# Optimization experiments

Measured on AMD Instinct MI355X. Metric: run time of the kernel, lower is better.

The kernel has to match this reference:

```python
import jax, jax.numpy as jnp
import numpy as np

B, DIM, NH = 2, 192, 6
HD = DIM // NH
S, H, W = 16, 32, 32
WS = (4, 4, 4)
WN = (S // WS[0], H // WS[1], W // WS[2])  # windows per axis (4,8,8)
NW = WN[0] * WN[1] * WN[2]                 # 256 windows
NWIN = WS[0] * WS[1] * WS[2]               # 64 tokens per window
SCALE = HD ** -0.5
TABLE = (2 * WS[0] - 1) * (2 * WS[1] - 1) * (2 * WS[2] - 1)  # 343


def _static_coords():
    # replicates torch __init__ base_coords / coords (shift_size=0, no padding)
    ls = np.linspace(-1, 1, S); lh = np.linspace(-1, 1, H); lw = np.linspace(-1, 1, W)
    img = np.stack(np.meshgrid(lw, lh, ls, indexing='ij'), 0)   # (3,W,H,S), ch=(x,y,z)
    img = img.transpose(0, 3, 2, 1)                              # (3,S,H,W)
    wr = img.reshape(3, WN[0], WS[0], WN[1], WS[1], WN[2], WS[2]).mean((2, 4, 6))
    wr = wr.reshape(1, 3, WN[0], 1, WN[1], 1, WN[2], 1)
    bs = np.arange(WS[0]) * 2.0 / (S - 1); bs = bs - bs.mean()
    bh = np.arange(WS[1]) * 2.0 / (H - 1); bh = bh - bh.mean()
    bw = np.arange(WS[2]) * 2.0 / (W - 1); bw = bw - bw.mean()
    es = np.tile(bs, WN[0]); eh = np.tile(bh, WN[1]); ew = np.tile(bw, WN[2])
    c = np.stack(np.meshgrid(ew, eh, es, indexing='ij'), 0).transpose(0, 3, 2, 1)
    c = c.reshape(1, 3, WN[0], WS[0], WN[1], WS[1], WN[2], WS[2])
    return (wr + c).astype(np.float32), c.astype(np.float32)

BASE_COORDS, REL_COORDS = _static_coords()


def _rel_pos_index():
    g = np.stack(np.meshgrid(np.arange(WS[0]), np.arange(WS[1]), np.arange(WS[2]), indexing='ij'))
    f = g.reshape(3, -1)
    r = (f[:, :, None] - f[:, None, :]).transpose(1, 2, 0)
    r[..., 0] += WS[0] - 1; r[..., 1] += WS[1] - 1; r[..., 2] += WS[2] - 1
    r[..., 0] *= 3 * WS[1] - 1   # faithful to source (3*ws_h-1 multiplier)
    r[..., 1] *= 2 * WS[1] - 1
    return r.sum(-1)  # (NWIN, NWIN) int

RPI = _rel_pos_index()


def conv1(x, w, b):  # 1x1x1 conv3d
    return jnp.einsum('bcshw,oc->boshw', x, w) + b[None, :, None, None, None]


def avg_pool_win(x):
    return x.reshape(x.shape[0], x.shape[1], WN[0], WS[0], WN[1], WS[1], WN[2], WS[2]).mean((3, 5, 7))


def leaky(x):
    return jnp.where(x >= 0, x, 0.01 * x)


def grid_sample_3d(inp, grid):
    # inp (N,C,D,H,W); grid (N,D,H,W,3) last dim = (x,y,z); align_corners=True, zeros padding
    N, C, D, Hh, Ww = inp.shape
    gx = (grid[..., 0] + 1.0) * (Ww - 1) / 2.0
    gy = (grid[..., 1] + 1.0) * (Hh - 1) / 2.0
    gz = (grid[..., 2] + 1.0) * (D - 1) / 2.0
    x0f = jnp.floor(gx); y0f = jnp.floor(gy); z0f = jnp.floor(gz)
    fx = gx - x0f; fy = gy - y0f; fz = gz - z0f
    x0 = x0f.astype(jnp.int32); y0 = y0f.astype(jnp.int32); z0 = z0f.astype(jnp.int32)

    def gat(iz, iy, ix):
        valid = ((iz >= 0) & (iz < D) & (iy >= 0) & (iy < Hh) & (ix >= 0) & (ix < Ww)).astype(inp.dtype)
        izc = jnp.clip(iz, 0, D - 1); iyc = jnp.clip(iy, 0, Hh - 1); ixc = jnp.clip(ix, 0, Ww - 1)
        vals = jax.vmap(lambda im, a, b, c: im[:, a, b, c])(inp, izc, iyc, ixc)  # (N,C,D,H,W)
        return vals * valid[:, None]

    out = jnp.zeros_like(inp)
    for dz, wz in ((0, 1.0 - fz), (1, fz)):
        for dy, wy in ((0, 1.0 - fy), (1, fy)):
            for dx, wx in ((0, 1.0 - fx), (1, fx)):
                out = out + gat(z0 + dz, y0 + dy, x0 + dx) * (wz * wy * wx)[:, None]
    return out


def to_windows(t):  # (B*NH, HD, S, H, W) -> (B*NW, NH, NWIN, HD)
    t = t.reshape(B, NH, HD, WN[0], WS[0], WN[1], WS[1], WN[2], WS[2])
    t = t.transpose(0, 3, 5, 7, 1, 4, 6, 8, 2)
    return t.reshape(B * NW, NH, NWIN, HD)


def setup_inputs() -> dict:
    key = jax.random.key(0)
    ks = jax.random.split(key, 8)
    return {
        'x': jax.random.normal(ks[0], (B, DIM, S, H, W), jnp.float32),
        'x_up': jax.random.normal(ks[1], (B, DIM, S, H, W), jnp.float32),
        'w_qkv': jax.random.normal(ks[2], (3 * DIM, DIM), jnp.float32) * 0.02,
        'b_qkv': jnp.zeros((3 * DIM,), jnp.float32),
        'w_off': jax.random.normal(ks[3], (NH * 3, DIM), jnp.float32) * 0.02,
        'b_off': jnp.zeros((NH * 3,), jnp.float32),
        'w_scale': jax.random.normal(ks[4], (NH * 3, DIM), jnp.float32) * 0.02,
        'b_scale': jnp.zeros((NH * 3,), jnp.float32),
        'w_proj': jax.random.normal(ks[5], (DIM, DIM), jnp.float32) * 0.02,
        'b_proj': jnp.zeros((DIM,), jnp.float32),
        'rpb_table': jax.random.normal(ks[6], (TABLE, NH), jnp.float32) * 0.02,
    }


def reference(x, x_up, w_qkv, b_qkv, w_off, b_off, w_scale, b_scale, w_proj, b_proj, rpb_table):
    # deformable sampling offsets / scales (avgpool -> leakyrelu -> 1x1 conv3d)
    pooled = leaky(avg_pool_win(x))
    off = conv1(pooled, w_off, b_off).reshape(B * NH, 3, WN[0], WN[1], WN[2])
    div = jnp.array([W // WS[2], H // WS[1], S // WS[0]], dtype=x.dtype).reshape(1, 3, 1, 1, 1)
    off = off / div
    sc = conv1(pooled, w_scale, b_scale).reshape(B * NH, 3, WN[0], WN[1], WN[2])
    coords = (jnp.asarray(BASE_COORDS)
              + jnp.asarray(REL_COORDS) * sc[:, :, :, None, :, None, :, None]
              + off[:, :, :, None, :, None, :, None])
    grid = coords.transpose(0, 2, 3, 4, 5, 6, 7, 1).reshape(B * NH, S, H, W, 3)

    # qkv 1x1 conv3d
    qkv = conv1(x, w_qkv, b_qkv).reshape(B, 3, NH, HD, S, H, W).transpose(1, 0, 2, 3, 4, 5, 6)
    q = qkv[0].reshape(B * NH, HD, S, H, W)
    k = qkv[1].reshape(B * NH, HD, S, H, W)
    v = qkv[2].reshape(B * NH, HD, S, H, W)

    k = grid_sample_3d(k, grid)
    v = grid_sample_3d(v, grid)

    qw, kw, vw = to_windows(q), to_windows(k), to_windows(v)
    rpb = rpb_table[jnp.asarray(RPI.reshape(-1))].reshape(NWIN, NWIN, NH).transpose(2, 0, 1)
    attn = jnp.einsum('wnqd,wnkd->wnqk', qw * SCALE, kw) + rpb[None]
    attn = jax.nn.softmax(attn, axis=-1)
    out = jnp.einsum('wnqk,wnkd->wnqd', attn, vw)

    out = out.reshape(B, WN[0], WN[1], WN[2], NH, WS[0], WS[1], WS[2], HD)
    out = out.transpose(0, 4, 8, 1, 5, 2, 6, 3, 7).reshape(B, DIM, S, H, W)
    return conv1(out, w_proj, b_proj)
```

## Files before the change

### kernel.cpp

```cpp
#include <hip/hip_runtime.h>
#include <math.h>

#define BB    2
#define DIMC  192
#define NHH   6
#define HDD   32
#define NPOS  16384
#define NWTOT 256
#define ATT_SCALE 0.17677669529663687f

typedef _Float16 f16x8 __attribute__((ext_vector_type(8)));
typedef _Float16 f16x4 __attribute__((ext_vector_type(4)));
typedef float f32x4 __attribute__((ext_vector_type(4)));

static __device__ __forceinline__ uint2 shfl_u2(uint2 v, int src) {
  uint2 r;
  r.x = (unsigned)__shfl((int)v.x, src, 64);
  r.y = (unsigned)__shfl((int)v.y, src, 64);
  return r;
}

__global__ void k_prep(const float* __restrict__ wq, const float* __restrict__ wp,
                       const float* __restrict__ rpb_g,
                       _Float16* __restrict__ whq, _Float16* __restrict__ whp,
                       _Float16* __restrict__ biasL) {
  int i = blockIdx.x * 256 + threadIdx.x;
  if (i < 576 * DIMC) {
    whq[i] = (_Float16)wq[i];
  } else if (i < 576 * DIMC + DIMC * DIMC) {
    int j = i - 576 * DIMC;
    whp[j] = (_Float16)wp[j];
  } else {
    int j = i - (576 * DIMC + DIMC * DIMC);
    if (j < 6 * 2 * 4 * 64 * 8) {
      int nh = j >> 12;
      int r = j & 4095;
      int hw = r >> 11;
      int r2 = r & 2047;
      int m = r2 >> 9;
      int lane = (r2 >> 3) & 63;
      int e = r2 & 7;
      int ni = e >> 2, ri = e & 3;
      int qt = (hw * 2 + ni) * 16 + (lane & 15);
      int kt = m * 16 + (lane >> 4) * 4 + ri;
      int d0 = (qt >> 4) - (kt >> 4) + 3;
      int d1 = ((qt >> 2) & 3) - ((kt >> 2) & 3) + 3;
      int d2 = (qt & 3) - (kt & 3) + 3;
      biasL[j] = (_Float16)rpb_g[(d0 * 11 + d1 * 7 + d2) * 6 + nh];
    }
  }
}

__global__ void k_transx(const float* __restrict__ x, _Float16* __restrict__ xt) {
  int idx = blockIdx.x * 256 + threadIdx.x;
  int p = idx & (NPOS - 1);
  int t = idx >> 14;
  int cseg = t % 24;
  int b = t / 24;
  if (b >= BB) return;
  const float* src = x + ((size_t)b * DIMC + cseg * 8) * NPOS + p;
  _Float16 v[8];
#pragma unroll
  for (int j = 0; j < 8; ++j) v[j] = (_Float16)src[(size_t)j * NPOS];
  *(uint4*)(xt + ((size_t)b * NPOS + p) * DIMC + cseg * 8) = *(uint4*)v;
}

__global__ __launch_bounds__(256) void k_poolsc(
    const _Float16* __restrict__ xt,
    const float* __restrict__ w_off, const float* __restrict__ b_off,
    const float* __restrict__ w_sc, const float* __restrict__ b_sc,
    float* __restrict__ off, float* __restrict__ sc) {
  __shared__ _Float16 X[64][208];
  __shared__ float P[192];
  int bid = blockIdx.x;
  int b = bid >> 8, win = bid & 255;
  int pbase = ((win >> 6) * 4) * 1024 + (((win >> 3) & 7) * 4) * 32 + (win & 7) * 4;
  int tid = threadIdx.x;
  {
    int tok = tid >> 2, part = tid & 3;
    int pp = pbase + (tok >> 4) * 1024 + ((tok >> 2) & 3) * 32 + (tok & 3);
    const _Float16* src = xt + ((size_t)b * NPOS + pp) * DIMC + part * 48;
#pragma unroll
    for (int s = 0; s < 6; ++s)
      *(uint4*)(&X[tok][part * 48 + s * 8]) = *(const uint4*)(src + s * 8);
  }
  __syncthreads();
  if (tid < DIMC) {
    float acc = 0.f;
#pragma unroll 8
    for (int t = 0; t < 64; ++t) acc += (float)X[t][tid];
    acc *= (1.f / 64.f);
    P[tid] = (acc >= 0.f) ? acc : 0.01f * acc;
  }
  __syncthreads();
  if (tid < 36) {
    int kind = (tid >= 18);
    int oo = kind ? tid - 18 : tid;
    const float* wrow = (kind ? w_sc : w_off) + oo * DIMC;
    float acc = (kind ? b_sc : b_off)[oo];
    for (int c = 0; c < DIMC; ++c) acc += wrow[c] * P[c];
    int nh = oo / 3, c3 = oo % 3;
    size_t dst = ((size_t)(b * NHH + nh) * 3 + c3) * NWTOT + win;
    if (!kind) {
      acc *= (c3 == 2) ? 0.25f : 0.125f;
      off[dst] = acc;
    } else {
      sc[dst] = acc;
    }
  }
}

template <int MODE>
__global__ __launch_bounds__(256) void k_gemm16(
    const _Float16* __restrict__ A, const float* __restrict__ bias,
    const _Float16* __restrict__ Bm, float* __restrict__ Y32,
    _Float16* __restrict__ qh, _Float16* __restrict__ kvh, int M, int N) {
  const int K = DIMC;
  int bz = blockIdx.z;
  int n0 = blockIdx.x * 128, m0 = blockIdx.y * 64;
  const _Float16* Bb = Bm + (size_t)bz * N * K;
  __shared__ _Float16 Al[64 * 64];
  __shared__ _Float16 Bl[128 * 64];
  int tid = threadIdx.x;
  int wave = tid >> 6, lane = tid & 63;
  int wm = wave >> 1, wn = wave & 1;
  int lrow = lane & 15, lkg = lane >> 4;
  f32x4 acc[2][4] = {};
  for (int k0 = 0; k0 < K; k0 += 64) {
    for (int c = tid; c < 512; c += 256) {
      int r = c >> 3, seg = c & 7;
      uint4 v = *(const uint4*)(A + (size_t)(m0 + r) * K + k0 + seg * 8);
      *(uint4*)((char*)Al + r * 128 + ((seg * 16) ^ ((r & 7) << 4))) = v;
    }
    for (int c = tid; c < 1024; c += 256) {
      int r = c >> 3, seg = c & 7;
      uint4 v = *(const uint4*)(Bb + (size_t)(n0 + r) * K + k0 + seg * 8);
      *(uint4*)((char*)Bl + r * 128 + ((seg * 16) ^ ((r & 7) << 4))) = v;
    }
    __syncthreads();
#pragma unroll
    for (int ks = 0; ks < 2; ++ks) {
      f16x8 af[2], bf[4];
#pragma unroll
      for (int mf = 0; mf < 2; ++mf) {
        int row = wm * 32 + mf * 16 + lrow;
        af[mf] = *(const f16x8*)((const char*)Al + row * 128 +
                                 ((ks * 64 + lkg * 16) ^ ((row & 7) << 4)));
      }
#pragma unroll
      for (int nf = 0; nf < 4; ++nf) {
        int row = wn * 64 + nf * 16 + lrow;
        bf[nf] = *(const f16x8*)((const char*)Bl + row * 128 +
                                 ((ks * 64 + lkg * 16) ^ ((row & 7) << 4)));
      }
#pragma unroll
      for (int mf = 0; mf < 2; ++mf)
#pragma unroll
        for (int nf = 0; nf < 4; ++nf)
          acc[mf][nf] = __builtin_amdgcn_mfma_f32_16x16x32_f16(af[mf], bf[nf], acc[mf][nf], 0, 0, 0);
    }
    __syncthreads();
  }
  int crow = lkg * 4, ccol = lrow;
#pragma unroll
  for (int mf = 0; mf < 2; ++mf)
#pragma unroll
    for (int nf = 0; nf < 4; ++nf) {
      int m = m0 + wm * 32 + mf * 16 + crow;
      int n = n0 + wn * 64 + nf * 16 + ccol;
      if (MODE == 1) {
        union { _Float16 h[4]; uint2 u; } pk;
#pragma unroll
        for (int r = 0; r < 4; ++r) pk.h[r] = (_Float16)(acc[mf][nf][r] + bias[m + r]);
        size_t rowi = (size_t)bz * NPOS + n;
        _Float16* dst;
        if (m < 192) dst = qh + rowi * 192 + m;
        else if (m < 384) { int mm = m - 192; dst = kvh + rowi * 384 + (mm >> 5) * 64 + (mm & 31); }
        else              { int mm = m - 384; dst = kvh + rowi * 384 + (mm >> 5) * 64 + 32 + (mm & 31); }
        *(uint2*)dst = pk.u;
      } else {
#pragma unroll
        for (int r = 0; r < 4; ++r)
          Y32[(size_t)bz * M * N + (size_t)(m + r) * N + n] = acc[mf][nf][r] + bias[m + r];
      }
    }
}

__global__ __launch_bounds__(128, 6) void k_sattn(
    const _Float16* __restrict__ qh, const _Float16* __restrict__ kvh,
    const float* __restrict__ off, const float* __restrict__ sc,
    const _Float16* __restrict__ biasL,
    _Float16* __restrict__ pin) {
  __shared__ char Kl[4096];
  __shared__ char Vt[4096];
  __shared__ int ci_lds[64][8];
  __shared__ _Float16 cw_lds[64][8];
  int bid = blockIdx.x;
  int swz = (bid & 7) * 384 + (bid >> 3);
  int nh = swz % 6;
  int t6 = swz / 6;
  int win = t6 & 255;
  int b = t6 >> 8;
  int bnh = b * NHH + nh;
  int tid = threadIdx.x;
  int lane = tid & 63, halfw = tid >> 6;
  int cl = lane & 15, g = lane >> 4;
  int pbase = ((win >> 6) * 4) * 1024 + (((win >> 3) & 7) * 4) * 32 + (win & 7) * 4;
  int prow = (cl >> 2) * 32 + (cl & 3);
  int n0 = halfw * 2;
  f16x8 qf[2];
  const _Float16* qbase = qh + ((size_t)b * NPOS) * 192 + nh * 32 + g * 8;
#pragma unroll
  for (int ni = 0; ni < 2; ++ni)
    qf[ni] = *(const f16x8*)(qbase + (size_t)(pbase + (n0 + ni) * 1024 + prow) * 192);
  f16x8 bm[4];
  {
    const _Float16* bl = biasL + ((size_t)(nh * 2 + halfw) * 4) * 512 + lane * 8;
#pragma unroll
    for (int m = 0; m < 4; ++m) bm[m] = *(const f16x8*)(bl + m * 512);
  }
  if (halfw == 0) {
    int tok = lane;
    int is = tok >> 4, ih = (tok >> 2) & 3, iw = tok & 3;
    int s = (win >> 6) * 4 + is, h = ((win >> 3) & 7) * 4 + ih, w = (win & 7) * 4 + iw;
    const float* ob = off + ((size_t)bnh * 3) * NWTOT + win;
    const float* sb = sc + ((size_t)bnh * 3) * NWTOT + win;
    float o0 = ob[0], o1 = ob[NWTOT], o2 = ob[2 * NWTOT];
    float s0 = sb[0], s1 = sb[NWTOT], s2 = sb[2 * NWTOT];
    float gxn = -1.f + 2.f * w / 31.f + ((2.f * iw - 3.f) / 31.f) * s0 + o0;
    float gyn = -1.f + 2.f * h / 31.f + ((2.f * ih - 3.f) / 31.f) * s1 + o1;
    float gzn = -1.f + 2.f * s / 15.f + ((2.f * is - 3.f) / 15.f) * s2 + o2;
    float gx = (gxn + 1.f) * 15.5f;
    float gy = (gyn + 1.f) * 15.5f;
    float gz = (gzn + 1.f) * 7.5f;
    float x0f = floorf(gx), y0f = floorf(gy), z0f = floorf(gz);
    float fx = gx - x0f, fy = gy - y0f, fz = gz - z0f;
    int x0 = (int)x0f, y0 = (int)y0f, z0 = (int)z0f;
    int n = 0;
    for (int dz = 0; dz < 2; ++dz)
      for (int dy = 0; dy < 2; ++dy)
        for (int dx = 0; dx < 2; ++dx) {
          int zz = z0 + dz, yy = y0 + dy, xx = x0 + dx;
          bool valid = (zz >= 0 && zz < 16 && yy >= 0 && yy < 32 && xx >= 0 && xx < 32);
          int zc = min(max(zz, 0), 15), yc = min(max(yy, 0), 31), xc = min(max(xx, 0), 31);
          float wgt = (dz ? fz : 1.f - fz) * (dy ? fy : 1.f - fy) * (dx ? fx : 1.f - fx);
          ci_lds[tok][n] = zc * 1024 + yc * 32 + xc;
          cw_lds[tok][n] = (_Float16)(valid ? wgt : 0.f);
          ++n;
        }
  }
  __syncthreads();
  int tbase = (halfw << 5) + (lane >> 3);
  int chk = lane & 7;
  int posr[8][4];
  _Float16 wr[8][4];
#pragma unroll
  for (int j = 0; j < 8; ++j)
#pragma unroll
    for (int tg = 0; tg < 4; ++tg) {
      int t = tbase + tg * 8;
      posr[j][tg] = ci_lds[t][j];
      wr[j][tg] = cw_lds[t][j];
    }
  const _Float16* kvbase = kvh + (size_t)b * NPOS * 384 + nh * 64 + chk * 8;
  f16x8 acc[4] = {};
#pragma unroll
  for (int j = 0; j < 8; ++j)
#pragma unroll
    for (int tg = 0; tg < 4; ++tg) {
      f16x8 v = *(const f16x8*)(kvbase + (size_t)posr[j][tg] * 384);
      _Float16 wv = wr[j][tg];
      f16x8 w8 = {wv, wv, wv, wv, wv, wv, wv, wv};
      acc[tg] += v * w8;
    }
  if (chk < 4) {
#pragma unroll
    for (int tg = 0; tg < 4; ++tg) {
      int t = tbase + tg * 8;
      *(f16x8*)(Kl + t * 64 + ((chk ^ ((t >> 1) & 3)) * 16)) = acc[tg];
    }
  } else {
    int cV = chk - 4;
#pragma unroll
    for (int tg = 0; tg < 4; ++tg) {
      int t = tbase + tg * 8;
#pragma unroll
      for (int e = 0; e < 8; ++e) {
        int hd = cV * 8 + e;
        *(_Float16*)(Vt + hd * 128 + ((t * 2) ^ ((hd & 7) << 4))) = acc[tg][e];
      }
    }
  }
  __syncthreads();
  f16x8 kf[4];
#pragma unroll
  for (int m = 0; m < 4; ++m) {
    int r = m * 16 + cl;
    kf[m] = *(const f16x8*)(Kl + r * 64 + ((g ^ ((r >> 1) & 3)) * 16));
  }
  f32x4 accT[4][2] = {};
  __builtin_amdgcn_s_setprio(1);
#pragma unroll
  for (int m = 0; m < 4; ++m)
#pragma unroll
    for (int ni = 0; ni < 2; ++ni)
      accT[m][ni] = __builtin_amdgcn_mfma_f32_16x16x32_f16(kf[m], qf[ni], accT[m][ni], 0, 0, 0);
  __builtin_amdgcn_s_setprio(0);
#pragma unroll
  for (int m = 0; m < 4; ++m)
#pragma unroll
    for (int ni = 0; ni < 2; ++ni)
#pragma unroll
      for (int ri = 0; ri < 4; ++ri)
        accT[m][ni][ri] = accT[m][ni][ri] * ATT_SCALE + (float)bm[m][ni * 4 + ri];
  uint2 pk[4][2];
#pragma unroll
  for (int ni = 0; ni < 2; ++ni) {
    float mx = -1e30f;
#pragma unroll
    for (int m = 0; m < 4; ++m)
#pragma unroll
      for (int ri = 0; ri < 4; ++ri) mx = fmaxf(mx, accT[m][ni][ri]);
    mx = fmaxf(mx, __shfl_xor(mx, 16));
    mx = fmaxf(mx, __shfl_xor(mx, 32));
    float sm = 0.f;
#pragma unroll
    for (int m = 0; m < 4; ++m)
#pragma unroll
      for (int ri = 0; ri < 4; ++ri) {
        float e = __expf(accT[m][ni][ri] - mx);
        accT[m][ni][ri] = e;
        sm += e;
      }
    sm += __shfl_xor(sm, 16);
    sm += __shfl_xor(sm, 32);
    float inv = 1.f / sm;
#pragma unroll
    for (int m = 0; m < 4; ++m) {
      union { _Float16 h[4]; uint2 u; } t;
#pragma unroll
      for (int ri = 0; ri < 4; ++ri) t.h[ri] = (_Float16)(accT[m][ni][ri] * inv);
      pk[m][ni] = t.u;
    }
  }
  int src_lo = ((g & 1) << 5) + cl;
  int src_hi = src_lo + 16;
  int msel = g >> 1;
  f32x4 accO[2][2] = {};
#pragma unroll
  for (int ks = 0; ks < 2; ++ks) {
    f16x8 va[2];
#pragma unroll
    for (int m2 = 0; m2 < 2; ++m2) {
      int hd = m2 * 16 + cl;
      va[m2] = *(const f16x8*)(Vt + hd * 128 + ((ks * 64 + g * 16) ^ ((hd & 7) << 4)));
    }
#pragma unroll
    for (int ni = 0; ni < 2; ++ni) {
      uint2 a0 = shfl_u2(pk[2 * ks][ni], src_lo);
      uint2 a1 = shfl_u2(pk[2 * ks + 1][ni], src_lo);
      uint2 b0 = shfl_u2(pk[2 * ks][ni], src_hi);
      uint2 b1 = shfl_u2(pk[2 * ks + 1][ni], src_hi);
      union { uint2 lohi[2]; f16x8 f; } u;
      u.lohi[0] = msel ? a1 : a0;
      u.lohi[1] = msel ? b1 : b0;
      __builtin_amdgcn_s_setprio(1);
#pragma unroll
      for (int m2 = 0; m2 < 2; ++m2)
        accO[m2][ni] = __builtin_amdgcn_mfma_f32_16x16x32_f16(va[m2], u.f, accO[m2][ni], 0, 0, 0);
      __builtin_amdgcn_s_setprio(0);
    }
  }
  _Float16* pb = pin + ((size_t)b * NPOS) * DIMC + nh * 32 + g * 4;
#pragma unroll
  for (int ni = 0; ni < 2; ++ni) {
    _Float16* dst = pb + (size_t)(pbase + (n0 + ni) * 1024 + prow) * DIMC;
#pragma unroll
    for (int m2 = 0; m2 < 2; ++m2) {
      union { _Float16 h[4]; uint2 u; } pkk;
#pragma unroll
      for (int r = 0; r < 4; ++r) pkk.h[r] = (_Float16)accO[m2][ni][r];
      *(uint2*)(dst + m2 * 16) = pkk.u;
    }
  }
}

extern "C" void kernel_launch(void* const* d_in, const int* in_sizes, int n_in,
                              void* d_out, int out_size, void* d_ws, size_t ws_size,
                              hipStream_t stream) {
  const float* x      = (const float*)d_in[0];
  const float* w_qkv  = (const float*)d_in[2];
  const float* b_qkv  = (const float*)d_in[3];
  const float* w_off  = (const float*)d_in[4];
  const float* b_off  = (const float*)d_in[5];
  const float* w_sc   = (const float*)d_in[6];
  const float* b_sc   = (const float*)d_in[7];
  const float* w_proj = (const float*)d_in[8];
  const float* b_proj = (const float*)d_in[9];
  const float* rpb    = (const float*)d_in[10];
  float* out = (float*)d_out;
  char* wsp = (char*)d_ws;

  _Float16* qhb = (_Float16*)wsp;                       wsp += (size_t)BB * NPOS * 192 * 2;
  _Float16* kvh = (_Float16*)wsp;                       wsp += (size_t)BB * NPOS * 384 * 2;
  _Float16* xt  = (_Float16*)wsp;                       wsp += (size_t)BB * NPOS * DIMC * 2;
  _Float16* pin = xt;
  _Float16* whq = (_Float16*)wsp;                       wsp += (size_t)576 * DIMC * 2;
  _Float16* whp = (_Float16*)wsp;                       wsp += (size_t)DIMC * DIMC * 2;
  _Float16* biasL = (_Float16*)wsp;                     wsp += (size_t)6 * 2 * 4 * 64 * 8 * 2;
  float* offb   = (float*)wsp;                          wsp += (size_t)BB * NHH * 3 * NWTOT * 4;
  float* scb    = (float*)wsp;

  k_prep<<<672, 256, 0, stream>>>(w_qkv, w_proj, rpb, whq, whp, biasL);
  k_transx<<<BB * 24 * NPOS / 256, 256, 0, stream>>>(x, xt);
  k_poolsc<<<BB * NWTOT, 256, 0, stream>>>(xt, w_off, b_off, w_sc, b_sc, offb, scb);
  k_gemm16<1><<<dim3(NPOS / 128, 576 / 64, BB), 256, 0, stream>>>(
      whq, b_qkv, xt, nullptr, qhb, kvh, 576, NPOS);
  k_sattn<<<3072, 128, 0, stream>>>(qhb, kvh, offb, scb, biasL, pin);
  k_gemm16<0><<<dim3(NPOS / 128, DIMC / 64, BB), 256, 0, stream>>>(
      whp, b_proj, pin, out, nullptr, nullptr, DIMC, NPOS);
}
```

Before: 86.52 us.

## Fuse input transpose into QKV GEMM loader and pool directly from fp32 input

Removes the separate k_transx kernel that converted x to a position-major fp16 copy. The QKV GEMM now reads the channel-major fp32 input directly, converting to fp16 and transposing into shared memory during the tile load. The pooling kernel reads fp32 windows straight from x with float4 loads. This drops one kernel launch and a full write and read of the intermediate, but each QKV tile is reloaded from fp32 across the 9 M-blocks, with strided global reads.

```diff
diff --git a/kernel.cpp b/kernel.cpp
--- a/kernel.cpp
+++ b/kernel.cpp
@@ -51,46 +51,28 @@
   }
 }
 
-__global__ void k_transx(const float* __restrict__ x, _Float16* __restrict__ xt) {
-  int idx = blockIdx.x * 256 + threadIdx.x;
-  int p = idx & (NPOS - 1);
-  int t = idx >> 14;
-  int cseg = t % 24;
-  int b = t / 24;
-  if (b >= BB) return;
-  const float* src = x + ((size_t)b * DIMC + cseg * 8) * NPOS + p;
-  _Float16 v[8];
-#pragma unroll
-  for (int j = 0; j < 8; ++j) v[j] = (_Float16)src[(size_t)j * NPOS];
-  *(uint4*)(xt + ((size_t)b * NPOS + p) * DIMC + cseg * 8) = *(uint4*)v;
-}
-
 __global__ __launch_bounds__(256) void k_poolsc(
-    const _Float16* __restrict__ xt,
+    const float* __restrict__ x,
     const float* __restrict__ w_off, const float* __restrict__ b_off,
     const float* __restrict__ w_sc, const float* __restrict__ b_sc,
     float* __restrict__ off, float* __restrict__ sc) {
-  __shared__ _Float16 X[64][208];
   __shared__ float P[192];
   int bid = blockIdx.x;
   int b = bid >> 8, win = bid & 255;
   int pbase = ((win >> 6) * 4) * 1024 + (((win >> 3) & 7) * 4) * 32 + (win & 7) * 4;
   int tid = threadIdx.x;
-  {
-    int tok = tid >> 2, part = tid & 3;
-    int pp = pbase + (tok >> 4) * 1024 + ((tok >> 2) & 3) * 32 + (tok & 3);
-    const _Float16* src = xt + ((size_t)b * NPOS + pp) * DIMC + part * 48;
-#pragma unroll
-    for (int s = 0; s < 6; ++s)
-      *(uint4*)(&X[tok][part * 48 + s * 8]) = *(const uint4*)(src + s * 8);
-  }
-  __syncthreads();
   if (tid < DIMC) {
-    float acc = 0.f;
-#pragma unroll 8
-    for (int t = 0; t < 64; ++t) acc += (float)X[t][tid];
-    acc *= (1.f / 64.f);
-    P[tid] = (acc >= 0.f) ? acc : 0.01f * acc;
+    const float* xb = x + ((size_t)(b * DIMC + tid)) * NPOS + pbase;
+    float s = 0.f;
+#pragma unroll
+    for (int iz = 0; iz < 4; ++iz)
+#pragma unroll
+      for (int iy = 0; iy < 4; ++iy) {
+        float4 v = *(const float4*)(xb + iz * 1024 + iy * 32);
+        s += v.x + v.y + v.z + v.w;
+      }
+    s *= (1.f / 64.f);
+    P[tid] = (s >= 0.f) ? s : 0.01f * s;
   }
   __syncthreads();
   if (tid < 36) {
@@ -113,12 +95,12 @@
 template <int MODE>
 __global__ __launch_bounds__(256) void k_gemm16(
     const _Float16* __restrict__ A, const float* __restrict__ bias,
-    const _Float16* __restrict__ Bm, float* __restrict__ Y32,
+    const _Float16* __restrict__ Bm, const float* __restrict__ X32,
+    float* __restrict__ Y32,
     _Float16* __restrict__ qh, _Float16* __restrict__ kvh, int M, int N) {
   const int K = DIMC;
   int bz = blockIdx.z;
   int n0 = blockIdx.x * 128, m0 = blockIdx.y * 64;
-  const _Float16* Bb = Bm + (size_t)bz * N * K;
   __shared__ _Float16 Al[64 * 64];
   __shared__ _Float16 Bl[128 * 64];
   int tid = threadIdx.x;
@@ -132,10 +114,23 @@
       uint4 v = *(const uint4*)(A + (size_t)(m0 + r) * K + k0 + seg * 8);
       *(uint4*)((char*)Al + r * 128 + ((seg * 16) ^ ((r & 7) << 4))) = v;
     }
-    for (int c = tid; c < 1024; c += 256) {
-      int r = c >> 3, seg = c & 7;
-      uint4 v = *(const uint4*)(Bb + (size_t)(n0 + r) * K + k0 + seg * 8);
-      *(uint4*)((char*)Bl + r * 128 + ((seg * 16) ^ ((r & 7) << 4))) = v;
+    if (MODE == 1) {
+      const float* Xb = X32 + (size_t)bz * DIMC * NPOS;
+      for (int c = tid; c < 1024; c += 256) {
+        int n = c & 127, kg = c >> 7;
+        const float* src = Xb + (size_t)(k0 + kg * 8) * NPOS + n0 + n;
+        union { _Float16 h[8]; uint4 u; } t;
+#pragma unroll
+        for (int j = 0; j < 8; ++j) t.h[j] = (_Float16)src[(size_t)j * NPOS];
+        *(uint4*)((char*)Bl + n * 128 + ((kg * 16) ^ ((n & 7) << 4))) = t.u;
+      }
+    } else {
+      const _Float16* Bb = Bm + (size_t)bz * N * K;
+      for (int c = tid; c < 1024; c += 256) {
+        int r = c >> 3, seg = c & 7;
+        uint4 v = *(const uint4*)(Bb + (size_t)(n0 + r) * K + k0 + seg * 8);
+        *(uint4*)((char*)Bl + r * 128 + ((seg * 16) ^ ((r & 7) << 4))) = v;
+      }
     }
     __syncthreads();
 #pragma unroll
@@ -403,8 +398,7 @@
 
   _Float16* qhb = (_Float16*)wsp;                       wsp += (size_t)BB * NPOS * 192 * 2;
   _Float16* kvh = (_Float16*)wsp;                       wsp += (size_t)BB * NPOS * 384 * 2;
-  _Float16* xt  = (_Float16*)wsp;                       wsp += (size_t)BB * NPOS * DIMC * 2;
-  _Float16* pin = xt;
+  _Float16* pin = (_Float16*)wsp;                       wsp += (size_t)BB * NPOS * DIMC * 2;
   _Float16* whq = (_Float16*)wsp;                       wsp += (size_t)576 * DIMC * 2;
   _Float16* whp = (_Float16*)wsp;                       wsp += (size_t)DIMC * DIMC * 2;
   _Float16* biasL = (_Float16*)wsp;                     wsp += (size_t)6 * 2 * 4 * 64 * 8 * 2;
@@ -412,11 +406,10 @@
   float* scb    = (float*)wsp;
 
   k_prep<<<672, 256, 0, stream>>>(w_qkv, w_proj, rpb, whq, whp, biasL);
-  k_transx<<<BB * 24 * NPOS / 256, 256, 0, stream>>>(x, xt);
-  k_poolsc<<<BB * NWTOT, 256, 0, stream>>>(xt, w_off, b_off, w_sc, b_sc, offb, scb);
   k_gemm16<1><<<dim3(NPOS / 128, 576 / 64, BB), 256, 0, stream>>>(
-      whq, b_qkv, xt, nullptr, qhb, kvh, 576, NPOS);
+      whq, b_qkv, nullptr, x, nullptr, qhb, kvh, 576, NPOS);
+  k_poolsc<<<BB * NWTOT, 256, 0, stream>>>(x, w_off, b_off, w_sc, b_sc, offb, scb);
   k_sattn<<<3072, 128, 0, stream>>>(qhb, kvh, offb, scb, biasL, pin);
   k_gemm16<0><<<dim3(NPOS / 128, DIMC / 64, BB), 256, 0, stream>>>(
-      whp, b_proj, pin, out, nullptr, nullptr, DIMC, NPOS);
-}
+      whp, b_proj, pin, nullptr, out, nullptr, nullptr, DIMC, NPOS);
+}
```

New measurement: 109.0 us. +26.0%, slower.
